# Optimization experiments

Measured on AMD Instinct MI355X. Metric: run time of the kernel, lower is better.

## Reference

```python
import jax, jax.numpy as jnp
import numpy as np
import math

S, B, H, NH = 2048, 2, 2048, 16
HD = H // NH
COEFF = 1.0  # layer_number = 1
NORM = math.sqrt(HD) * COEFF
MASK_VAL = -10000.0


def setup_inputs() -> dict:
    key = jax.random.key(0)
    ks = jax.random.split(key, 4)
    hidden_states = jax.random.normal(ks[0], (S, B, H), dtype=jnp.float32)
    # causal mask: True = masked (Megatron convention)
    attention_mask = jnp.triu(jnp.ones((S, S), dtype=bool), k=1)[None, None]
    w_qkv = jax.random.normal(ks[1], (H, 3 * H), dtype=jnp.float32) * (1.0 / math.sqrt(H))
    b_qkv = jnp.zeros((3 * H,), dtype=jnp.float32)
    w_dense = jax.random.normal(ks[2], (H, H), dtype=jnp.float32) * (1.0 / math.sqrt(H))
    b_dense = jnp.zeros((H,), dtype=jnp.float32)
    return {"hidden_states": hidden_states, "attention_mask": attention_mask,
            "w_qkv": w_qkv, "b_qkv": b_qkv, "w_dense": w_dense, "b_dense": b_dense}


def reference(hidden_states, attention_mask, w_qkv, b_qkv, w_dense, b_dense):
    s, b, h = hidden_states.shape
    # QKV projection: [s, b, 3h] -> [s, b, nh, 3*hd] -> split
    mixed = hidden_states @ w_qkv + b_qkv
    mixed = mixed.reshape(s, b, NH, 3 * HD)
    q, k, v = jnp.split(mixed, 3, axis=-1)  # each [s, b, nh, hd]
    # raw scores scaled by 1/(sqrt(hd)*coeff)  -> [b, nh, s_q, s_k]
    scores = jnp.einsum('sbnd,tbnd->bnst', q, k) / NORM
    # fused scale-mask-softmax in fp32 with scale=coeff (net 1/sqrt(hd))
    scores32 = scores.astype(jnp.float32) * COEFF
    scores32 = jnp.where(attention_mask, MASK_VAL, scores32)
    probs = jax.nn.softmax(scores32, axis=-1).astype(hidden_states.dtype)
    # dropout p=0.0 -> identity
    context = jnp.einsum('bnst,tbnd->sbnd', probs, v).reshape(s, b, h)
    # row-parallel dense with skip_bias_add: bias returned separately
    output = context @ w_dense
    return output, b_dense
```

## Files before the change

### kernel.cpp

```cpp
#include <hip/hip_runtime.h>
#include <hip/hip_bf16.h>

constexpr int S   = 2048;
constexpr int B   = 2;
constexpr int H   = 2048;
constexpr int NH  = 16;
constexpr int HD  = 128;
constexpr int K3H = 3 * H;
constexpr float SCALE2 = 0.08838834764831845f * 1.4426950408889634f;
constexpr float MSHIFT = 12.0f;

typedef __attribute__((ext_vector_type(8))) short short8;
typedef __attribute__((ext_vector_type(4))) float f32x4;

__device__ __forceinline__ ushort f2b(float f) {
  uint u = __float_as_uint(f);
  return (ushort)((u + 0x7fffu + ((u >> 16) & 1u)) >> 16);
}

__device__ __forceinline__ f32x4 mfma16(short8 a, short8 b, f32x4 c) {
  return __builtin_amdgcn_mfma_f32_16x16x32_bf16(a, b, c, 0, 0, 0);
}

__device__ __forceinline__ void gld16(const ushort* g, ushort* l) {
  __builtin_amdgcn_global_load_lds((const __attribute__((address_space(1))) void*)g,
                                   (__attribute__((address_space(3))) void*)l,
                                   16, 0, 0);
}

__global__ __launch_bounds__(256) void cast_bf16(const float* __restrict__ src,
                                                 ushort* __restrict__ dst, int n) {
  int i = (blockIdx.x * 256 + threadIdx.x) * 4;
  if (i >= n) return;
  float4 v = *(const float4*)(src + i);
  ushort4 o;
  o.x = f2b(v.x); o.y = f2b(v.y); o.z = f2b(v.z); o.w = f2b(v.w);
  *(ushort4*)(dst + i) = o;
}

__global__ __launch_bounds__(256) void transpose_cast(const float* __restrict__ src,
                                                      ushort* __restrict__ dst,
                                                      int R, int C) {
  __shared__ ushort tile[32][33];
  int c0 = blockIdx.x * 32, r0 = blockIdx.y * 32;
  int tx = threadIdx.x, ty = threadIdx.y;
#pragma unroll
  for (int i = 0; i < 4; i++) {
    int r = r0 + ty + i * 8;
    tile[ty + i * 8][tx] = f2b(src[(size_t)r * C + c0 + tx]);
  }
  __syncthreads();
#pragma unroll
  for (int i = 0; i < 4; i++) {
    int c = c0 + ty + i * 8;
    dst[(size_t)c * R + r0 + tx] = tile[tx][ty + i * 8];
  }
}

template <int MODE>
__global__ __launch_bounds__(512, 2) void gemm_bt(const ushort* __restrict__ A,
                                                  const ushort* __restrict__ Bt,
                                                  const float* __restrict__ bias,
                                                  void* __restrict__ out0,
                                                  void* __restrict__ out1,
                                                  int M, int N, int K) {
  __shared__ __align__(16) ushort lds_a[3][256 * 64];
  __shared__ __align__(16) ushort lds_b[3][128 * 64];
  const int tid  = threadIdx.x;
  const int wave = tid >> 6, lane = tid & 63;
  const int quad = lane >> 4, l15 = lane & 15;
  const int wm = wave >> 1, wn = wave & 1;
  const int m0 = blockIdx.y * 256, n0 = blockIdx.x * 128;

  f32x4 acc[4][4] = {};

  const int srow   = tid >> 3;
  const int schunk = (tid & 7) ^ (srow & 7);
  const ushort* gaS = A  + (size_t)(m0 + srow) * K + schunk * 8;
  const ushort* gbS = Bt + (size_t)(n0 + srow) * K + schunk * 8;
  const size_t rs64 = (size_t)64 * K;

  const int fsw = l15 & 7;

  auto stageT = [&](int kt, int bf) {
    const size_t ko = (size_t)kt * 64;
#pragma unroll
    for (int h = 0; h < 4; h++)
      gld16(gaS + (size_t)h * rs64 + ko, &lds_a[bf][(h * 512 + wave * 64) * 8]);
#pragma unroll
    for (int h = 0; h < 2; h++)
      gld16(gbS + (size_t)h * rs64 + ko, &lds_b[bf][(h * 512 + wave * 64) * 8]);
  };

  const int NT = K >> 6;

  stageT(0, 0);
  stageT(1, 1);
  asm volatile("s_waitcnt vmcnt(6)" ::: "memory");
  __builtin_amdgcn_s_barrier();

  int bf = 0;
  for (int kt = 0; kt < NT; ++kt) {
    const bool pf = (kt + 2 < NT);
    const int nf = (kt + 2) % 3;

    short8 af[2][4], bq[2][4];
#pragma unroll
    for (int kk = 0; kk < 2; ++kk) {
#pragma unroll
      for (int mt = 0; mt < 4; mt++)
        af[kk][mt] = *(const short8*)&lds_a[bf][((wm * 64 + mt * 16 + l15) * 8 + ((kk * 4 + quad) ^ fsw)) * 8];
#pragma unroll
      for (int nt = 0; nt < 4; nt++)
        bq[kk][nt] = *(const short8*)&lds_b[bf][((wn * 64 + nt * 16 + l15) * 8 + ((kk * 4 + quad) ^ fsw)) * 8];
    }

    if (pf) stageT(kt + 2, nf);

    __builtin_amdgcn_s_setprio(1);
#pragma unroll
    for (int kk = 0; kk < 2; ++kk)
#pragma unroll
      for (int mt = 0; mt < 4; mt++)
#pragma unroll
        for (int nt = 0; nt < 4; nt++)
          acc[mt][nt] = mfma16(af[kk][mt], bq[kk][nt], acc[mt][nt]);
    __builtin_amdgcn_s_setprio(0);

    if (kt + 1 < NT) {
      if (pf) asm volatile("s_waitcnt vmcnt(6)" ::: "memory");
      else    asm volatile("s_waitcnt vmcnt(0)" ::: "memory");
      __builtin_amdgcn_s_barrier();
    }
    bf = (bf + 1 == 3) ? 0 : bf + 1;
  }

  if (MODE == 1) {
#pragma unroll
    for (int nt = 0; nt < 4; nt++) {
      const int col = n0 + wn * 64 + nt * 16 + l15;
      const int nh  = col / 384;
      const int rem = col - nh * 384;
      const float bv = bias[col];
      if (rem < 256) {
        ushort* qk = (ushort*)out0;
#pragma unroll
        for (int mt = 0; mt < 4; mt++) {
          const int rb = m0 + wm * 64 + mt * 16 + quad * 4;
#pragma unroll
          for (int i = 0; i < 4; i++)
            qk[((size_t)(rb + i) * NH + nh) * 256 + rem] = f2b(acc[mt][nt][i] + bv);
        }
      } else {
        ushort* vt = (ushort*)out1;
        const size_t colbase = ((size_t)nh * 128 + (rem - 256)) * S;
#pragma unroll
        for (int mt = 0; mt < 4; mt++) {
          const int rb = m0 + wm * 64 + mt * 16 + quad * 4;
#pragma unroll
          for (int i = 0; i < 4; i++) {
            const int row = rb + i;
            vt[(size_t)(row & 1) * ((size_t)NH * 128 * S) + colbase + (row >> 1)]
                = f2b(acc[mt][nt][i] + bv);
          }
        }
      }
    }
  } else {
    float* Co = (float*)out0;
#pragma unroll
    for (int mt = 0; mt < 4; mt++)
#pragma unroll
      for (int nt = 0; nt < 4; nt++) {
        const int col = n0 + wn * 64 + nt * 16 + l15;
#pragma unroll
        for (int i = 0; i < 4; i++) {
          const int row = m0 + wm * 64 + mt * 16 + quad * 4 + i;
          Co[(size_t)row * N + col] = acc[mt][nt][i];
        }
      }
  }
}

__global__ __launch_bounds__(512) void flash_attn(const ushort* __restrict__ qkb,
                                                  const ushort* __restrict__ VtG,
                                                  ushort* __restrict__ ctxb) {
  __shared__ ushort Ks[2][64 * 128];
  __shared__ ushort Vt[2][128 * 64];
  __shared__ ushort Pls[8][16 * 64];

  const int tid  = threadIdx.x;
  const int wave = tid >> 6, lane = tid & 63;
  const int quad = lane >> 4, l15 = lane & 15;
  const int jj = blockIdx.x;
  const int nh = blockIdx.y, b = blockIdx.z;
  const int stA = jj, stB = 15 - jj;
  const int nA = 2 * jj + 2;
  constexpr int TOT = 34;

  ushort* Pw = Pls[wave];

  const int ktRow = tid >> 4;
  const int kCol  = (tid & 15) ^ (ktRow & 15);
  const ushort* kS = qkb + (((size_t)(ktRow * B + b) * NH + nh) * 256 + 128 + kCol * 8);
  const int vdRow = tid >> 3;
  const int vCol  = (tid & 7) ^ (vdRow & 7);
  const ushort* vS = VtG + ((size_t)(b * NH + nh) * 128 + vdRow) * (size_t)S + vCol * 8;

  const size_t kRowStep32 = (size_t)32 * B * NH * 256;
  const size_t vRowStep64 = (size_t)64 * S;
  const size_t kTileStep  = (size_t)64 * B * NH * 256;

  auto stageTile = [&](int kt, int nxt) {
    const size_t ko = (size_t)kt * kTileStep;
    const int vo = kt * 64;
    gld16(kS + ko, &Ks[nxt][(wave * 64) * 8]);
    gld16(kS + ko + kRowStep32, &Ks[nxt][(512 + wave * 64) * 8]);
    gld16(vS + vo, &Vt[nxt][(wave * 64) * 8]);
    gld16(vS + vo + vRowStep64, &Vt[nxt][(512 + wave * 64) * 8]);
  };

  short8 qf[4];
  int q0 = stA * 128;
  {
    const ushort* qPtr = qkb + (((size_t)((q0 + wave * 16 + l15) * B + b) * NH + nh) * 256 + quad * 8);
#pragma unroll
    for (int ks = 0; ks < 4; ks++) qf[ks] = *(const short8*)(qPtr + ks * 32);
  }

  float l_r[4];
  f32x4 acc_o[8];
#pragma unroll
  for (int i = 0; i < 4; i++) l_r[i] = 0.0f;
#pragma unroll
  for (int j = 0; j < 8; j++) acc_o[j] = (f32x4){0.f, 0.f, 0.f, 0.f};

  stageTile(0, 0);
  __syncthreads();

  for (int it = 0; it < TOT; it++) {
    const int buf = it & 1;
    const int kt = (it < nA) ? it : it - nA;
    const int t0 = kt * 64;

    if (it + 1 < TOT)
      stageTile((it + 1 < nA) ? it + 1 : it + 1 - nA, buf ^ 1);

    f32x4 sa[4];
#pragma unroll
    for (int nt = 0; nt < 4; nt++) sa[nt] = (f32x4){0.f, 0.f, 0.f, 0.f};
#pragma unroll
    for (int ks = 0; ks < 4; ks++) {
#pragma unroll
      for (int nt = 0; nt < 4; nt++) {
        const int gs = (ks * 4 + quad) ^ l15;
        short8 bq = *(const short8*)&Ks[buf][((nt * 16 + l15) * 16 + gs) * 8];
        sa[nt] = mfma16(qf[ks], bq, sa[nt]);
      }
    }

    const int qw0 = q0 + wave * 16;
    const bool diag = (t0 + 63 > qw0);
#pragma unroll
    for (int i = 0; i < 4; i++) {
      const int qg = qw0 + quad * 4 + i;
      const int prow = quad * 4 + i;
      float lacc = l_r[i];
#pragma unroll
      for (int nt = 0; nt < 4; nt++) {
        float e = fmaf(sa[nt][i], SCALE2, -MSHIFT);
        if (diag) {
          const int tg = t0 + nt * 16 + l15;
          if (tg > qg) e = -1e30f;
        }
        const float p = exp2f(e);
        lacc += p;
        const int gs = (nt * 2 + (l15 >> 3)) ^ (prow & 7);
        Pw[prow * 64 + gs * 8 + (l15 & 7)] = f2b(p);
      }
      l_r[i] = lacc;
    }

#pragma unroll
    for (int ks2 = 0; ks2 < 2; ks2++) {
      const int pg = (ks2 * 4 + quad) ^ (l15 & 7);
      short8 a2 = *(const short8*)&Pw[l15 * 64 + pg * 8];
#pragma unroll
      for (int j = 0; j < 8; j++) {
        const int gs = (ks2 * 4 + quad) ^ (l15 & 7);
        short8 b2 = *(const short8*)&Vt[buf][((j * 16 + l15) * 8 + gs) * 8];
        acc_o[j] = mfma16(a2, b2, acc_o[j]);
      }
    }

    if (it == nA - 1) {
#pragma unroll
      for (int i = 0; i < 4; i++) {
        float ls = l_r[i];
#pragma unroll
        for (int off = 1; off < 16; off <<= 1) ls += __shfl_xor(ls, off);
        const float inv = 1.0f / ls;
        const int qg = q0 + wave * 16 + quad * 4 + i;
        ushort* dst = ctxb + ((size_t)qg * B + b) * H + nh * HD;
#pragma unroll
        for (int j = 0; j < 8; j++)
          dst[j * 16 + l15] = f2b(acc_o[j][i] * inv);
      }
      q0 = stB * 128;
      const ushort* qPtr = qkb + (((size_t)((q0 + wave * 16 + l15) * B + b) * NH + nh) * 256 + quad * 8);
#pragma unroll
      for (int ks = 0; ks < 4; ks++) qf[ks] = *(const short8*)(qPtr + ks * 32);
#pragma unroll
      for (int i = 0; i < 4; i++) l_r[i] = 0.0f;
#pragma unroll
      for (int j = 0; j < 8; j++) acc_o[j] = (f32x4){0.f, 0.f, 0.f, 0.f};
    }

    __syncthreads();
  }

#pragma unroll
  for (int i = 0; i < 4; i++) {
    float ls = l_r[i];
#pragma unroll
    for (int off = 1; off < 16; off <<= 1) ls += __shfl_xor(ls, off);
    const float inv = 1.0f / ls;
    const int qg = q0 + wave * 16 + quad * 4 + i;
    ushort* dst = ctxb + ((size_t)qg * B + b) * H + nh * HD;
#pragma unroll
    for (int j = 0; j < 8; j++)
      dst[j * 16 + l15] = f2b(acc_o[j][i] * inv);
  }
}

extern "C" void kernel_launch(void* const* d_in, const int* in_sizes, int n_in,
                              void* d_out, int out_size, void* d_ws, size_t ws_size,
                              hipStream_t stream) {
  (void)in_sizes; (void)n_in; (void)out_size; (void)ws_size;
  const float* hs     = (const float*)d_in[0];
  const float* wqkv   = (const float*)d_in[2];
  const float* bqkv   = (const float*)d_in[3];
  const float* wdense = (const float*)d_in[4];
  const float* bdense = (const float*)d_in[5];
  float* out = (float*)d_out;

  ushort* Xb      = (ushort*)d_ws;
  ushort* WqkvT   = Xb      + (size_t)S * B * H;
  ushort* WdenseT = WqkvT   + (size_t)H * K3H;
  ushort* qkb     = WdenseT + (size_t)H * H;
  ushort* VtG     = qkb     + (size_t)S * B * NH * 256;
  ushort* ctxb    = VtG     + (size_t)B * NH * HD * S;

  cast_bf16<<<dim3((S * B * H) / 1024), dim3(256), 0, stream>>>(hs, Xb, S * B * H);
  transpose_cast<<<dim3(K3H / 32, H / 32), dim3(32, 8), 0, stream>>>(wqkv, WqkvT, H, K3H);
  transpose_cast<<<dim3(H / 32, H / 32), dim3(32, 8), 0, stream>>>(wdense, WdenseT, H, H);

  gemm_bt<1><<<dim3(K3H / 128, (S * B) / 256), dim3(512), 0, stream>>>(
      Xb, WqkvT, bqkv, qkb, VtG, S * B, K3H, H);

  flash_attn<<<dim3(8, NH, B), dim3(512), 0, stream>>>(qkb, VtG, ctxb);

  gemm_bt<0><<<dim3(H / 128, (S * B) / 256), dim3(512), 0, stream>>>(
      ctxb, WdenseT, nullptr, out, nullptr, S * B, H, H);

  hipMemcpyAsync(out + (size_t)S * B * H, bdense, H * sizeof(float),
                 hipMemcpyDeviceToDevice, stream);
}
```

Before: 391.4 us.

## Use simple 128x128 single-buffered GEMM for QKV projection and prioritize attention MFMAs

Splits the templated GEMM into a QKV-specific kernel and a dense kernel. The QKV kernel becomes a simpler 256-thread, 128x128-tile, single-buffered loop with two barriers per k-step, which doubles the grid to about 1536 blocks, presumably for better occupancy and wave balance. The dense GEMM keeps the triple-buffered 256x128 pipeline. Flash attention also raises wave priority around its MFMA blocks. The simpler QKV kernel gives up load/compute overlap, so it risks more time stalled on loads.

```diff
diff --git a/kernel.cpp b/kernel.cpp
--- a/kernel.cpp
+++ b/kernel.cpp
@@ -57,13 +57,91 @@
   }
 }
 
-template <int MODE>
-__global__ __launch_bounds__(512, 2) void gemm_bt(const ushort* __restrict__ A,
-                                                  const ushort* __restrict__ Bt,
-                                                  const float* __restrict__ bias,
-                                                  void* __restrict__ out0,
-                                                  void* __restrict__ out1,
-                                                  int M, int N, int K) {
+__global__ __launch_bounds__(256) void gemm_qkv(const ushort* __restrict__ A,
+                                                const ushort* __restrict__ Bt,
+                                                const float* __restrict__ bias,
+                                                ushort* __restrict__ out0,
+                                                ushort* __restrict__ out1,
+                                                int M, int N, int K) {
+  __shared__ ushort lds_a[128 * 64];
+  __shared__ ushort lds_b[128 * 64];
+  const int tid  = threadIdx.x;
+  const int wave = tid >> 6, lane = tid & 63;
+  const int quad = lane >> 4, l15 = lane & 15;
+  const int wr = wave >> 1, wc = wave & 1;
+  const int m0 = blockIdx.y * 128, n0 = blockIdx.x * 128;
+
+  f32x4 acc[4][4] = {};
+
+  const int srow   = tid >> 3;
+  const int schunk = (tid & 7) ^ (srow & 7);
+  const ushort* gaS = A  + (size_t)(m0 + srow) * K + schunk * 8;
+  const ushort* gbS = Bt + (size_t)(n0 + srow) * K + schunk * 8;
+
+  const int fsw = l15 & 7;
+
+  const int nk = K >> 6;
+  for (int kt = 0; kt < nk; kt++) {
+    const int ko = kt * 64;
+#pragma unroll
+    for (int j = 0; j < 4; j++) {
+      gld16(gaS + (size_t)(j * 32) * K + ko, &lds_a[(j * 256 + wave * 64) * 8]);
+      gld16(gbS + (size_t)(j * 32) * K + ko, &lds_b[(j * 256 + wave * 64) * 8]);
+    }
+    __syncthreads();
+
+#pragma unroll
+    for (int ks = 0; ks < 2; ks++) {
+      short8 af[4], bq[4];
+#pragma unroll
+      for (int mt = 0; mt < 4; mt++)
+        af[mt] = *(const short8*)&lds_a[((wr * 64 + mt * 16 + l15) * 8 + ((ks * 4 + quad) ^ fsw)) * 8];
+#pragma unroll
+      for (int nt = 0; nt < 4; nt++)
+        bq[nt] = *(const short8*)&lds_b[((wc * 64 + nt * 16 + l15) * 8 + ((ks * 4 + quad) ^ fsw)) * 8];
+#pragma unroll
+      for (int mt = 0; mt < 4; mt++)
+#pragma unroll
+        for (int nt = 0; nt < 4; nt++)
+          acc[mt][nt] = mfma16(af[mt], bq[nt], acc[mt][nt]);
+    }
+    __syncthreads();
+  }
+
+#pragma unroll
+  for (int nt = 0; nt < 4; nt++) {
+    const int col = n0 + wc * 64 + nt * 16 + l15;
+    const int nh  = col / 384;
+    const int rem = col - nh * 384;
+    const float bv = bias[col];
+    if (rem < 256) {
+#pragma unroll
+      for (int mt = 0; mt < 4; mt++) {
+        const int rb = m0 + wr * 64 + mt * 16 + quad * 4;
+#pragma unroll
+        for (int i = 0; i < 4; i++)
+          out0[((size_t)(rb + i) * NH + nh) * 256 + rem] = f2b(acc[mt][nt][i] + bv);
+      }
+    } else {
+      const size_t colbase = ((size_t)nh * 128 + (rem - 256)) * S;
+#pragma unroll
+      for (int mt = 0; mt < 4; mt++) {
+        const int rb = m0 + wr * 64 + mt * 16 + quad * 4;
+#pragma unroll
+        for (int i = 0; i < 4; i++) {
+          const int row = rb + i;
+          out1[(size_t)(row & 1) * ((size_t)NH * 128 * S) + colbase + (row >> 1)]
+              = f2b(acc[mt][nt][i] + bv);
+        }
+      }
+    }
+  }
+}
+
+__global__ __launch_bounds__(512, 2) void gemm_dense(const ushort* __restrict__ A,
+                                                     const ushort* __restrict__ Bt,
+                                                     float* __restrict__ Co,
+                                                     int M, int N, int K) {
   __shared__ __align__(16) ushort lds_a[3][256 * 64];
   __shared__ __align__(16) ushort lds_b[3][128 * 64];
   const int tid  = threadIdx.x;
@@ -135,51 +213,17 @@
     bf = (bf + 1 == 3) ? 0 : bf + 1;
   }
 
-  if (MODE == 1) {
+#pragma unroll
+  for (int mt = 0; mt < 4; mt++)
 #pragma unroll
     for (int nt = 0; nt < 4; nt++) {
       const int col = n0 + wn * 64 + nt * 16 + l15;
-      const int nh  = col / 384;
-      const int rem = col - nh * 384;
-      const float bv = bias[col];
-      if (rem < 256) {
-        ushort* qk = (ushort*)out0;
-#pragma unroll
-        for (int mt = 0; mt < 4; mt++) {
-          const int rb = m0 + wm * 64 + mt * 16 + quad * 4;
-#pragma unroll
-          for (int i = 0; i < 4; i++)
-            qk[((size_t)(rb + i) * NH + nh) * 256 + rem] = f2b(acc[mt][nt][i] + bv);
-        }
-      } else {
-        ushort* vt = (ushort*)out1;
-        const size_t colbase = ((size_t)nh * 128 + (rem - 256)) * S;
-#pragma unroll
-        for (int mt = 0; mt < 4; mt++) {
-          const int rb = m0 + wm * 64 + mt * 16 + quad * 4;
-#pragma unroll
-          for (int i = 0; i < 4; i++) {
-            const int row = rb + i;
-            vt[(size_t)(row & 1) * ((size_t)NH * 128 * S) + colbase + (row >> 1)]
-                = f2b(acc[mt][nt][i] + bv);
-          }
-        }
-      }
-    }
-  } else {
-    float* Co = (float*)out0;
-#pragma unroll
-    for (int mt = 0; mt < 4; mt++)
-#pragma unroll
-      for (int nt = 0; nt < 4; nt++) {
-        const int col = n0 + wn * 64 + nt * 16 + l15;
-#pragma unroll
-        for (int i = 0; i < 4; i++) {
-          const int row = m0 + wm * 64 + mt * 16 + quad * 4 + i;
-          Co[(size_t)row * N + col] = acc[mt][nt][i];
-        }
-      }
-  }
+#pragma unroll
+      for (int i = 0; i < 4; i++) {
+        const int row = m0 + wm * 64 + mt * 16 + quad * 4 + i;
+        Co[(size_t)row * N + col] = acc[mt][nt][i];
+      }
+    }
 }
 
 __global__ __launch_bounds__(512) void flash_attn(const ushort* __restrict__ qkb,
@@ -249,6 +293,7 @@
     f32x4 sa[4];
 #pragma unroll
     for (int nt = 0; nt < 4; nt++) sa[nt] = (f32x4){0.f, 0.f, 0.f, 0.f};
+    __builtin_amdgcn_s_setprio(1);
 #pragma unroll
     for (int ks = 0; ks < 4; ks++) {
 #pragma unroll
@@ -258,6 +303,7 @@
         sa[nt] = mfma16(qf[ks], bq, sa[nt]);
       }
     }
+    __builtin_amdgcn_s_setprio(0);
 
     const int qw0 = q0 + wave * 16;
     const bool diag = (t0 + 63 > qw0);
@@ -281,6 +327,7 @@
       l_r[i] = lacc;
     }
 
+    __builtin_amdgcn_s_setprio(1);
 #pragma unroll
     for (int ks2 = 0; ks2 < 2; ks2++) {
       const int pg = (ks2 * 4 + quad) ^ (l15 & 7);
@@ -292,6 +339,7 @@
         acc_o[j] = mfma16(a2, b2, acc_o[j]);
       }
     }
+    __builtin_amdgcn_s_setprio(0);
 
     if (it == nA - 1) {
 #pragma unroll
@@ -355,13 +403,13 @@
   transpose_cast<<<dim3(K3H / 32, H / 32), dim3(32, 8), 0, stream>>>(wqkv, WqkvT, H, K3H);
   transpose_cast<<<dim3(H / 32, H / 32), dim3(32, 8), 0, stream>>>(wdense, WdenseT, H, H);
 
-  gemm_bt<1><<<dim3(K3H / 128, (S * B) / 256), dim3(512), 0, stream>>>(
+  gemm_qkv<<<dim3(K3H / 128, (S * B) / 128), dim3(256), 0, stream>>>(
       Xb, WqkvT, bqkv, qkb, VtG, S * B, K3H, H);
 
   flash_attn<<<dim3(8, NH, B), dim3(512), 0, stream>>>(qkb, VtG, ctxb);
 
-  gemm_bt<0><<<dim3(H / 128, (S * B) / 256), dim3(512), 0, stream>>>(
-      ctxb, WdenseT, nullptr, out, nullptr, S * B, H, H);
+  gemm_dense<<<dim3(H / 128, (S * B) / 256), dim3(512), 0, stream>>>(
+      ctxb, WdenseT, out, S * B, H, H);
 
   hipMemcpyAsync(out + (size_t)S * B * H, bdense, H * sizeof(float),
                  hipMemcpyDeviceToDevice, stream);
```

After: 408.3 us, median of 2. +4.3%, slower.
